# Performance work log

Hardware: AMD Instinct MI355X
Metric: run time of the kernel (lower is better)

Reference implementation:

```python
import jax, jax.numpy as jnp
import numpy as np

ALPHA = 0.9     # projection strength
EPS = 1e-3      # Lyapunov positive-definite regularizer (lyapunov_eps)
B, D, H = 32768, 512, 64


def setup_inputs() -> dict:
    key = jax.random.key(0)
    ks = jax.random.split(key, 8)
    def w(k, shape, fan_in):
        return jax.random.normal(k, shape, jnp.float32) * (1.0 / fan_in) ** 0.5
    return dict(
        x=jax.random.normal(ks[0], (B, D), jnp.float32),
        # dynamics MLP f(x): D -> 64 -> 64 -> D
        W1=w(ks[1], (D, H), D), b1=jnp.zeros((H,), jnp.float32),
        W2=w(ks[2], (H, H), H), b2=jnp.zeros((H,), jnp.float32),
        W3=w(ks[3], (H, D), H), b3=jnp.zeros((D,), jnp.float32),
        # Lyapunov MLP V(z): D -> 64 -> 64 -> 1 (+ eps*||z||^2)
        V1=w(ks[4], (D, H), D), c1=jnp.zeros((H,), jnp.float32),
        V2=w(ks[5], (H, H), H), c2=jnp.zeros((H,), jnp.float32),
        V3=w(ks[6], (H, 1), H), c3=jnp.zeros((1,), jnp.float32),
    )


def reference(x, W1, b1, W2, b2, W3, b3, V1, c1, V2, c2, V3, c3):
    def fnet(xx):  # nominal dynamics: [B,D] -> [B,D]
        h = jax.nn.relu(xx @ W1 + b1)
        h = jax.nn.relu(h @ W2 + b2)
        return h @ W3 + b3

    def vnet(z):  # Lyapunov candidate: [B,D] -> [B]
        h = jax.nn.relu(z @ V1 + c1)
        h = jax.nn.relu(h @ V2 + c2)
        return (h @ V3 + c3)[..., 0] + EPS * jnp.sum(z * z, axis=-1)

    def lyap_sum(xx):
        v = vnet(fnet(xx))
        return jnp.sum(v), v

    # grad_v replicates the in-forward lyapunov.backward(...): dV(f(x))/dx, shape [B,D]
    (_, lyap), grad_v = jax.value_and_grad(lyap_sum, has_aux=True)(x)

    f = fnet(x)                                   # [B, D]
    dot = jnp.sum(grad_v * grad_v, axis=-1)       # bmm(gv, fv): per-sample <grad_v, grad_v>
    denom = jnp.sum(grad_v * grad_v)              # global .pow(2).sum() over all elements
    orth = jax.nn.relu(dot + ALPHA * lyap) / denom  # [B]
    return f - orth[:, None] * grad_v             # diag_embed(orth) @ grad_v
```

## Files before the change

kernel.cpp:

```cpp
#include <hip/hip_runtime.h>

#define ALPHA_C 0.9f
#define EPS_C 1e-3f

typedef unsigned short u16;
typedef __attribute__((ext_vector_type(8))) short short8;
typedef __attribute__((ext_vector_type(4))) short short4v;
typedef __attribute__((ext_vector_type(4))) float f32x4;
#define MFMA(a, b, c) __builtin_amdgcn_mfma_f32_16x16x32_bf16(a, b, c, 0, 0, 0)
#define LDS_FENCE() asm volatile("" ::: "memory")

__device__ __forceinline__ u16 f2bf(float f) {
  union { float f; unsigned u; } v; v.f = f;
  unsigned u = v.u;
  u += 0x7FFFu + ((u >> 16) & 1u);
  return (u16)(u >> 16);
}
__device__ __forceinline__ float bf2f(u16 h) {
  union { unsigned u; float f; } v; v.u = ((unsigned)h) << 16;
  return v.f;
}

__global__ __launch_bounds__(256) void k_conv(
    const float* __restrict__ W1, const float* __restrict__ W2, const float* __restrict__ W3,
    const float* __restrict__ V1, const float* __restrict__ V2,
    u16* __restrict__ PW1T, u16* __restrict__ PW1n, u16* __restrict__ PV1T, u16* __restrict__ PV1n,
    u16* __restrict__ PW3T, u16* __restrict__ PW3n, u16* __restrict__ PW2T, u16* __restrict__ PW2n,
    u16* __restrict__ PV2T, u16* __restrict__ PV2n) {
  int i = blockIdx.x * 256 + threadIdx.x;
  {
    int k = i >> 6, j = i & 63;
    u16 b = f2bf(W1[i]);
    PW1T[((((j >> 4) * 16 + (k >> 5)) * 4 + ((k & 31) >> 3)) * 16 + (j & 15)) * 8 + (k & 7)] = b;
    PW1n[((((k >> 4) * 2 + (j >> 5)) * 4 + ((j & 31) >> 3)) * 16 + (k & 15)) * 8 + (j & 7)] = b;
    u16 c = f2bf(V1[i]);
    PV1T[((((j >> 4) * 16 + (k >> 5)) * 4 + ((k & 31) >> 3)) * 16 + (j & 15)) * 8 + (k & 7)] = c;
    PV1n[((((k >> 4) * 2 + (j >> 5)) * 4 + ((j & 31) >> 3)) * 16 + (k & 15)) * 8 + (j & 7)] = c;
  }
  {
    int k = i >> 9, n = i & 511;
    u16 b = f2bf(W3[i]);
    PW3T[((((n >> 4) * 2 + (k >> 5)) * 4 + ((k & 31) >> 3)) * 16 + (n & 15)) * 8 + (k & 7)] = b;
    PW3n[((((k >> 4) * 16 + (n >> 5)) * 4 + ((n & 31) >> 3)) * 16 + (k & 15)) * 8 + (n & 7)] = b;
  }
  if (i < 4096) {
    int k = i >> 6, j = i & 63;
    u16 b = f2bf(W2[i]);
    PW2T[((((j >> 4) * 2 + (k >> 5)) * 4 + ((k & 31) >> 3)) * 16 + (j & 15)) * 8 + (k & 7)] = b;
    PW2n[((((k >> 4) * 2 + (j >> 5)) * 4 + ((j & 31) >> 3)) * 16 + (k & 15)) * 8 + (j & 7)] = b;
    u16 c = f2bf(V2[i]);
    PV2T[((((j >> 4) * 2 + (k >> 5)) * 4 + ((k & 31) >> 3)) * 16 + (j & 15)) * 8 + (k & 7)] = c;
    PV2n[((((k >> 4) * 2 + (j >> 5)) * 4 + ((j & 31) >> 3)) * 16 + (k & 15)) * 8 + (j & 7)] = c;
  }
}

__global__ __launch_bounds__(256, 2) void k_fused(
    const float* __restrict__ x,
    const u16* __restrict__ PW1T, const float* __restrict__ b1,
    const u16* __restrict__ PW2T, const float* __restrict__ b2,
    const u16* __restrict__ PW3T, const float* __restrict__ b3,
    const u16* __restrict__ PV1T, const float* __restrict__ c1,
    const u16* __restrict__ PV2T, const u16* __restrict__ PV2n, const float* __restrict__ c2,
    const float* __restrict__ V3, const float* __restrict__ c3,
    const u16* __restrict__ PV1n, const u16* __restrict__ PW3n,
    const u16* __restrict__ PW2n, const u16* __restrict__ PW1n,
    u16* __restrict__ FP, u16* __restrict__ T2P,
    float* __restrict__ NUM, float* __restrict__ DP) {
  __shared__ u16 H1s[64 * 72];
  __shared__ u16 H2s[64 * 72];
  __shared__ u16 S2s[64 * 72];
  __shared__ u16 As[64 * 136];
  __shared__ float dred[4];
  const int tid = threadIdx.x;
  const int lane = tid & 63, w = tid >> 6, q = lane >> 4, r = lane & 15;
  const int m0 = blockIdx.x * 64;
  const int arow = w * 16 + r;
  const int strip = blockIdx.x * 4 + w;
  const int h = lane >> 5, c4 = lane & 31;
  const float* xbase = x + (size_t)(m0 + w * 16) * 512;

  f32x4 acc1[4] = {};
  float4 xr0[8], xr1[8];

#define LOAD_X(regs, kc)                                                        \
  _Pragma("unroll") for (int it = 0; it < 8; ++it)                              \
    regs[it] = *(const float4*)&xbase[(it * 2 + h) * 512 + (kc) * 128 + c4 * 4];

#define STAGE_X(regs)                                                           \
  _Pragma("unroll") for (int it = 0; it < 8; ++it) {                            \
    float4 v = regs[it];                                                        \
    short4v s4;                                                                 \
    s4[0] = (short)f2bf(v.x); s4[1] = (short)f2bf(v.y);                         \
    s4[2] = (short)f2bf(v.z); s4[3] = (short)f2bf(v.w);                         \
    *(short4v*)&As[(w * 16 + it * 2 + h) * 136 + c4 * 4] = s4;                  \
  }

#define MFMA_X(kc)                                                              \
  _Pragma("unroll") for (int ks = 0; ks < 4; ++ks) {                            \
    short8 a = *(const short8*)&As[arow * 136 + ks * 32 + q * 8];               \
    _Pragma("unroll") for (int t = 0; t < 4; ++t) {                             \
      short8 b = *(const short8*)&PW1T[((t * 16 + (kc) * 4 + ks) * 64 + lane) * 8]; \
      acc1[t] = MFMA(a, b, acc1[t]);                                            \
    }                                                                           \
  }

  LOAD_X(xr0, 0)
  STAGE_X(xr0) LDS_FENCE(); LOAD_X(xr1, 1) MFMA_X(0) LDS_FENCE();
  STAGE_X(xr1) LDS_FENCE(); LOAD_X(xr0, 2) MFMA_X(1) LDS_FENCE();
  STAGE_X(xr0) LDS_FENCE(); LOAD_X(xr1, 3) MFMA_X(2) LDS_FENCE();
  STAGE_X(xr1) LDS_FENCE(); MFMA_X(3)

  #pragma unroll
  for (int t = 0; t < 4; ++t) {
    int col = t * 16 + r; float bv = b1[col];
    #pragma unroll
    for (int g = 0; g < 4; ++g) {
      float hh = acc1[t][g] + bv; hh = hh > 0.f ? hh : 0.f;
      H1s[(w * 16 + q * 4 + g) * 72 + col] = f2bf(hh);
    }
  }
  LDS_FENCE();

  f32x4 acc2[4] = {};
  #pragma unroll
  for (int ks = 0; ks < 2; ++ks) {
    short8 a = *(const short8*)&H1s[arow * 72 + ks * 32 + q * 8];
    #pragma unroll
    for (int t = 0; t < 4; ++t) {
      short8 b = *(const short8*)&PW2T[((t * 2 + ks) * 64 + lane) * 8];
      acc2[t] = MFMA(a, b, acc2[t]);
    }
  }
  #pragma unroll
  for (int t = 0; t < 4; ++t) {
    int col = t * 16 + r; float bv = b2[col];
    #pragma unroll
    for (int g = 0; g < 4; ++g) {
      float hh = acc2[t][g] + bv; hh = hh > 0.f ? hh : 0.f;
      H2s[(w * 16 + q * 4 + g) * 72 + col] = f2bf(hh);
    }
  }
  LDS_FENCE();

  f32x4 g1acc[4] = {};
  float ssq[4] = {0.f, 0.f, 0.f, 0.f};
  #pragma unroll 1
  for (int nc = 0; nc < 4; ++nc) {
    f32x4 facc[8] = {};
    #pragma unroll
    for (int ks = 0; ks < 2; ++ks) {
      short8 a = *(const short8*)&H2s[arow * 72 + ks * 32 + q * 8];
      #pragma unroll
      for (int t = 0; t < 8; ++t) {
        short8 b = *(const short8*)&PW3T[(((nc * 8 + t) * 2 + ks) * 64 + lane) * 8];
        facc[t] = MFMA(a, b, facc[t]);
      }
    }
    #pragma unroll
    for (int t = 0; t < 8; ++t) {
      float bv = b3[nc * 128 + t * 16 + r];
      short4v s4;
      #pragma unroll
      for (int g = 0; g < 4; ++g) {
        float v = facc[t][g] + bv;
        ssq[g] += v * v;
        u16 bb = f2bf(v);
        As[(w * 16 + q * 4 + g) * 136 + t * 16 + r] = bb;
        s4[g] = (short)bb;
      }
      *(short4v*)&FP[(size_t)(((strip * 4 + nc) * 8 + t) * 64 + lane) * 4] = s4;
    }
    LDS_FENCE();
    #pragma unroll
    for (int ks = 0; ks < 4; ++ks) {
      short8 a = *(const short8*)&As[arow * 136 + ks * 32 + q * 8];
      #pragma unroll
      for (int t = 0; t < 4; ++t) {
        short8 b = *(const short8*)&PV1T[((t * 16 + nc * 4 + ks) * 64 + lane) * 8];
        g1acc[t] = MFMA(a, b, g1acc[t]);
      }
    }
    LDS_FENCE();
  }

  f32x4 g1v[4];
  #pragma unroll
  for (int t = 0; t < 4; ++t) {
    int col = t * 16 + r; float cv = c1[col];
    #pragma unroll
    for (int g = 0; g < 4; ++g) {
      float v = g1acc[t][g] + cv; v = v > 0.f ? v : 0.f;
      g1v[t][g] = v;
      S2s[(w * 16 + q * 4 + g) * 72 + col] = f2bf(v);
    }
  }
  LDS_FENCE();
  f32x4 g2acc[4] = {};
  #pragma unroll
  for (int ks = 0; ks < 2; ++ks) {
    short8 a = *(const short8*)&S2s[arow * 72 + ks * 32 + q * 8];
    #pragma unroll
    for (int t = 0; t < 4; ++t) {
      short8 b = *(const short8*)&PV2T[((t * 2 + ks) * 64 + lane) * 8];
      g2acc[t] = MFMA(a, b, g2acc[t]);
    }
  }
  float tot[4] = {0.f, 0.f, 0.f, 0.f};
  #pragma unroll
  for (int t = 0; t < 4; ++t) {
    int col = t * 16 + r;
    float c2v = c2[col], v3v = V3[col];
    #pragma unroll
    for (int g = 0; g < 4; ++g) {
      float pre = g2acc[t][g] + c2v;
      float g2 = pre > 0.f ? pre : 0.f;
      S2s[(w * 16 + q * 4 + g) * 72 + col] = pre > 0.f ? f2bf(v3v) : (u16)0;
      tot[g] += g2 * v3v;
    }
  }
  LDS_FENCE();
  f32x4 s2acc[4] = {};
  #pragma unroll
  for (int ks = 0; ks < 2; ++ks) {
    short8 a = *(const short8*)&S2s[arow * 72 + ks * 32 + q * 8];
    #pragma unroll
    for (int t = 0; t < 4; ++t) {
      short8 b = *(const short8*)&PV2n[((t * 2 + ks) * 64 + lane) * 8];
      s2acc[t] = MFMA(a, b, s2acc[t]);
    }
  }
  #pragma unroll
  for (int t = 0; t < 4; ++t) {
    int col = t * 16 + r;
    #pragma unroll
    for (int g = 0; g < 4; ++g) {
      float sv = g1v[t][g] > 0.f ? s2acc[t][g] : 0.f;
      S2s[(w * 16 + q * 4 + g) * 72 + col] = f2bf(sv);
    }
  }
  LDS_FENCE();
  float c3v = c3[0];
  float lyap_row[4];
  #pragma unroll
  for (int g = 0; g < 4; ++g) {
    float s = tot[g] + EPS_C * ssq[g];
    s += __shfl_xor(s, 1); s += __shfl_xor(s, 2); s += __shfl_xor(s, 4); s += __shfl_xor(s, 8);
    lyap_row[g] = s + c3v;
  }

  asm volatile("s_waitcnt vmcnt(0)" ::: "memory");

  f32x4 t3acc[4] = {};
  #pragma unroll 1
  for (int nc = 0; nc < 4; ++nc) {
    f32x4 uacc[8] = {};
    #pragma unroll
    for (int ks = 0; ks < 2; ++ks) {
      short8 a = *(const short8*)&S2s[arow * 72 + ks * 32 + q * 8];
      #pragma unroll
      for (int t = 0; t < 8; ++t) {
        short8 b = *(const short8*)&PV1n[(((nc * 8 + t) * 2 + ks) * 64 + lane) * 8];
        uacc[t] = MFMA(a, b, uacc[t]);
      }
    }
    #pragma unroll
    for (int t = 0; t < 8; ++t) {
      short4v f4 = *(const short4v*)&FP[(size_t)(((strip * 4 + nc) * 8 + t) * 64 + lane) * 4];
      #pragma unroll
      for (int g = 0; g < 4; ++g) {
        As[(w * 16 + q * 4 + g) * 136 + t * 16 + r] =
            f2bf(uacc[t][g] + 2.f * EPS_C * bf2f((u16)f4[g]));
      }
    }
    LDS_FENCE();
    #pragma unroll
    for (int ks = 0; ks < 4; ++ks) {
      short8 a = *(const short8*)&As[arow * 136 + ks * 32 + q * 8];
      #pragma unroll
      for (int t = 0; t < 4; ++t) {
        short8 b = *(const short8*)&PW3n[((t * 16 + nc * 4 + ks) * 64 + lane) * 8];
        t3acc[t] = MFMA(a, b, t3acc[t]);
      }
    }
    LDS_FENCE();
  }
  #pragma unroll
  for (int t = 0; t < 4; ++t) {
    int col = t * 16 + r;
    #pragma unroll
    for (int g = 0; g < 4; ++g) {
      int addr = (w * 16 + q * 4 + g) * 72 + col;
      u16 h2 = H2s[addr];
      H2s[addr] = h2 ? f2bf(t3acc[t][g]) : (u16)0;
    }
  }
  LDS_FENCE();
  f32x4 t2acc[4] = {};
  #pragma unroll
  for (int ks = 0; ks < 2; ++ks) {
    short8 a = *(const short8*)&H2s[arow * 72 + ks * 32 + q * 8];
    #pragma unroll
    for (int t = 0; t < 4; ++t) {
      short8 b = *(const short8*)&PW2n[((t * 2 + ks) * 64 + lane) * 8];
      t2acc[t] = MFMA(a, b, t2acc[t]);
    }
  }
  #pragma unroll
  for (int t = 0; t < 4; ++t) {
    int col = t * 16 + r;
    #pragma unroll
    for (int g = 0; g < 4; ++g) {
      int addr = (w * 16 + q * 4 + g) * 72 + col;
      u16 h1 = H1s[addr];
      H1s[addr] = h1 ? f2bf(t2acc[t][g]) : (u16)0;
    }
  }
  LDS_FENCE();
  short8 v0 = *(const short8*)&H1s[arow * 72 + 0 + q * 8];
  short8 v1 = *(const short8*)&H1s[arow * 72 + 32 + q * 8];
  *(short8*)&T2P[(size_t)((strip * 2 + 0) * 64 + lane) * 8] = v0;
  *(short8*)&T2P[(size_t)((strip * 2 + 1) * 64 + lane) * 8] = v1;
  float ssq2[4] = {0.f, 0.f, 0.f, 0.f};
  #pragma unroll 1
  for (int nc = 0; nc < 4; ++nc) {
    f32x4 acc[8] = {};
    #pragma unroll
    for (int t = 0; t < 8; ++t) {
      short8 b0 = *(const short8*)&PW1n[(((nc * 8 + t) * 2 + 0) * 64 + lane) * 8];
      short8 b1 = *(const short8*)&PW1n[(((nc * 8 + t) * 2 + 1) * 64 + lane) * 8];
      acc[t] = MFMA(v0, b0, acc[t]);
      acc[t] = MFMA(v1, b1, acc[t]);
    }
    #pragma unroll
    for (int t = 0; t < 8; ++t)
      #pragma unroll
      for (int g = 0; g < 4; ++g) ssq2[g] += acc[t][g] * acc[t][g];
  }
  float totw = 0.f;
  #pragma unroll
  for (int g = 0; g < 4; ++g) {
    float s = ssq2[g];
    s += __shfl_xor(s, 1); s += __shfl_xor(s, 2); s += __shfl_xor(s, 4); s += __shfl_xor(s, 8);
    if (r == 0) {
      int rowg = m0 + w * 16 + q * 4 + g;
      float nm = s + ALPHA_C * lyap_row[g];
      NUM[rowg] = nm > 0.f ? nm : 0.f;
    }
    s += __shfl_xor(s, 16); s += __shfl_xor(s, 32);
    totw += s;
  }
  if (lane == 0) dred[w] = totw;
  __syncthreads();
  if (tid == 0) atomicAdd(&DP[blockIdx.x & 255], dred[0] + dred[1] + dred[2] + dred[3]);
}

__global__ __launch_bounds__(256) void k_out(
    const u16* __restrict__ T2P, const u16* __restrict__ PW1n,
    const u16* __restrict__ FP, const float* __restrict__ NUM, const float* __restrict__ DP,
    float* __restrict__ out) {
  __shared__ float red[256];
  const int tid = threadIdx.x;
  const int lane = tid & 63, w = tid >> 6, q = lane >> 4, r = lane & 15;
  const int m0 = blockIdx.x * 64;
  const int strip = blockIdx.x * 4 + w;
  red[tid] = DP[tid];
  __syncthreads();
  for (int s = 128; s >= 1; s >>= 1) {
    if (tid < s) red[tid] += red[tid + s];
    __syncthreads();
  }
  const float inv_denom = 1.f / red[0];
  float sc[4];
  #pragma unroll
  for (int g = 0; g < 4; ++g) sc[g] = NUM[m0 + w * 16 + q * 4 + g] * inv_denom;
  short8 a0 = *(const short8*)&T2P[(size_t)((strip * 2 + 0) * 64 + lane) * 8];
  short8 a1 = *(const short8*)&T2P[(size_t)((strip * 2 + 1) * 64 + lane) * 8];
  #pragma unroll 1
  for (int nc = 0; nc < 4; ++nc) {
    f32x4 acc[8] = {};
    #pragma unroll
    for (int t = 0; t < 8; ++t) {
      short8 b0 = *(const short8*)&PW1n[(((nc * 8 + t) * 2 + 0) * 64 + lane) * 8];
      short8 b1 = *(const short8*)&PW1n[(((nc * 8 + t) * 2 + 1) * 64 + lane) * 8];
      acc[t] = MFMA(a0, b0, acc[t]);
      acc[t] = MFMA(a1, b1, acc[t]);
    }
    #pragma unroll
    for (int t = 0; t < 8; ++t) {
      short4v f4 = *(const short4v*)&FP[(size_t)(((strip * 4 + nc) * 8 + t) * 64 + lane) * 4];
      #pragma unroll
      for (int g = 0; g < 4; ++g) {
        out[(size_t)(m0 + w * 16 + q * 4 + g) * 512 + nc * 128 + t * 16 + r] =
            bf2f((u16)f4[g]) - sc[g] * acc[t][g];
      }
    }
  }
}

extern "C" void kernel_launch(void* const* d_in, const int* in_sizes, int n_in,
                              void* d_out, int out_size, void* d_ws, size_t ws_size,
                              hipStream_t stream) {
  const float* x  = (const float*)d_in[0];
  const float* W1 = (const float*)d_in[1];
  const float* b1 = (const float*)d_in[2];
  const float* W2 = (const float*)d_in[3];
  const float* b2 = (const float*)d_in[4];
  const float* W3 = (const float*)d_in[5];
  const float* b3 = (const float*)d_in[6];
  const float* V1 = (const float*)d_in[7];
  const float* c1 = (const float*)d_in[8];
  const float* V2 = (const float*)d_in[9];
  const float* c2 = (const float*)d_in[10];
  const float* V3 = (const float*)d_in[11];
  const float* c3 = (const float*)d_in[12];
  float* out = (float*)d_out;

  u16* FP = (u16*)d_ws;
  float* NUM = (float*)(FP + 16777216);
  float* DP  = NUM + 32768;
  u16* T2P  = (u16*)(DP + 256);
  u16* PW1T = T2P + 2097152;
  u16* PW1n = PW1T + 32768;
  u16* PV1T = PW1n + 32768;
  u16* PV1n = PV1T + 32768;
  u16* PW3T = PV1n + 32768;
  u16* PW3n = PW3T + 32768;
  u16* PW2T = PW3n + 32768;
  u16* PW2n = PW2T + 4096;
  u16* PV2T = PW2n + 4096;
  u16* PV2n = PV2T + 4096;

  hipMemsetAsync(DP, 0, 256 * sizeof(float), stream);

  k_conv<<<128, 256, 0, stream>>>(W1, W2, W3, V1, V2,
                                  PW1T, PW1n, PV1T, PV1n, PW3T, PW3n,
                                  PW2T, PW2n, PV2T, PV2n);
  k_fused<<<512, 256, 0, stream>>>(x, PW1T, b1, PW2T, b2, PW3T, b3, PV1T, c1,
                                   PV2T, PV2n, c2, V3, c3, PV1n, PW3n, PW2n, PW1n,
                                   FP, T2P, NUM, DP);
  k_out<<<512, 256, 0, stream>>>(T2P, PW1n, FP, NUM, DP, out);
}
```

Baseline: 178.3 us.

## Software-pipeline weight fragment loads into registers and stage output stores via LDS

Weight B-fragments for each MFMA stage are prefetched into two rotating register banks (bA/bB), so the global loads for the next chunk are issued while the current chunk's MFMAs run. This applies across all GEMM stages of the fused kernel and to the output kernel. The output kernel also stages results in shared memory so it can write each row with coalesced float4 stores. The DP memset is folded into the weight-conversion kernel, removing one launch. The cost is more registers, which could limit occupancy, plus extra LDS in k_out.

```diff
diff --git a/kernel.cpp b/kernel.cpp
--- a/kernel.cpp
+++ b/kernel.cpp
@@ -26,8 +26,9 @@
     const float* __restrict__ V1, const float* __restrict__ V2,
     u16* __restrict__ PW1T, u16* __restrict__ PW1n, u16* __restrict__ PV1T, u16* __restrict__ PV1n,
     u16* __restrict__ PW3T, u16* __restrict__ PW3n, u16* __restrict__ PW2T, u16* __restrict__ PW2n,
-    u16* __restrict__ PV2T, u16* __restrict__ PV2n) {
+    u16* __restrict__ PV2T, u16* __restrict__ PV2n, float* __restrict__ DP) {
   int i = blockIdx.x * 256 + threadIdx.x;
+  if (i < 256) DP[i] = 0.f;
   {
     int k = i >> 6, j = i & 63;
     u16 b = f2bf(W1[i]);
@@ -53,6 +54,10 @@
     PV2n[((((k >> 4) * 2 + (j >> 5)) * 4 + ((j & 31) >> 3)) * 16 + (k & 15)) * 8 + (j & 7)] = c;
   }
 }
+
+#define LDG8(dst, P, FRAG)                                                      \
+  _Pragma("unroll") for (int j = 0; j < 8; ++j)                                 \
+    dst[j] = *(const short8*)&P[((size_t)(FRAG) * 64 + lane) * 8];
 
 __global__ __launch_bounds__(256, 2) void k_fused(
     const float* __restrict__ x,
@@ -79,36 +84,42 @@
   const int h = lane >> 5, c4 = lane & 31;
   const float* xbase = x + (size_t)(m0 + w * 16) * 512;
 
+  short8 bA[8], bB[8];
+
   f32x4 acc1[4] = {};
-  float4 xr0[8], xr1[8];
-
-#define LOAD_X(regs, kc)                                                        \
-  _Pragma("unroll") for (int it = 0; it < 8; ++it)                              \
-    regs[it] = *(const float4*)&xbase[(it * 2 + h) * 512 + (kc) * 128 + c4 * 4];
-
-#define STAGE_X(regs)                                                           \
-  _Pragma("unroll") for (int it = 0; it < 8; ++it) {                            \
-    float4 v = regs[it];                                                        \
-    short4v s4;                                                                 \
-    s4[0] = (short)f2bf(v.x); s4[1] = (short)f2bf(v.y);                         \
-    s4[2] = (short)f2bf(v.z); s4[3] = (short)f2bf(v.w);                         \
-    *(short4v*)&As[(w * 16 + it * 2 + h) * 136 + c4 * 4] = s4;                  \
-  }
-
-#define MFMA_X(kc)                                                              \
-  _Pragma("unroll") for (int ks = 0; ks < 4; ++ks) {                            \
-    short8 a = *(const short8*)&As[arow * 136 + ks * 32 + q * 8];               \
-    _Pragma("unroll") for (int t = 0; t < 4; ++t) {                             \
-      short8 b = *(const short8*)&PW1T[((t * 16 + (kc) * 4 + ks) * 64 + lane) * 8]; \
-      acc1[t] = MFMA(a, b, acc1[t]);                                            \
+  float4 xr[8];
+  #pragma unroll
+  for (int it = 0; it < 8; ++it)
+    xr[it] = *(const float4*)&xbase[(it * 2 + h) * 512 + c4 * 4];
+  LDG8(bA, PW1T, (j & 3) * 16 + 0 * 4 + (j >> 2));
+
+#define A1_STEP(kc, LAST)                                                       \
+  {                                                                             \
+    _Pragma("unroll") for (int it = 0; it < 8; ++it) {                          \
+      float4 v = xr[it]; short4v s4;                                            \
+      s4[0] = (short)f2bf(v.x); s4[1] = (short)f2bf(v.y);                       \
+      s4[2] = (short)f2bf(v.z); s4[3] = (short)f2bf(v.w);                       \
+      *(short4v*)&As[(w * 16 + it * 2 + h) * 136 + c4 * 4] = s4;                \
     }                                                                           \
-  }
-
-  LOAD_X(xr0, 0)
-  STAGE_X(xr0) LDS_FENCE(); LOAD_X(xr1, 1) MFMA_X(0) LDS_FENCE();
-  STAGE_X(xr1) LDS_FENCE(); LOAD_X(xr0, 2) MFMA_X(1) LDS_FENCE();
-  STAGE_X(xr0) LDS_FENCE(); LOAD_X(xr1, 3) MFMA_X(2) LDS_FENCE();
-  STAGE_X(xr1) LDS_FENCE(); MFMA_X(3)
+    LDS_FENCE();                                                                \
+    if (!LAST) {                                                                \
+      _Pragma("unroll") for (int it = 0; it < 8; ++it)                          \
+        xr[it] = *(const float4*)&xbase[(it * 2 + h) * 512 + (kc + 1) * 128 + c4 * 4]; \
+    }                                                                           \
+    LDG8(bB, PW1T, (j & 3) * 16 + (kc) * 4 + 2 + (j >> 2));       \
+    short8 a0 = *(const short8*)&As[arow * 136 + 0 * 32 + q * 8];               \
+    short8 a1 = *(const short8*)&As[arow * 136 + 1 * 32 + q * 8];               \
+    _Pragma("unroll") for (int t = 0; t < 4; ++t) acc1[t] = MFMA(a0, bA[t], acc1[t]); \
+    _Pragma("unroll") for (int t = 0; t < 4; ++t) acc1[t] = MFMA(a1, bA[4 + t], acc1[t]); \
+    if (!LAST) { LDG8(bA, PW1T, (j & 3) * 16 + (kc + 1) * 4 + (j >> 2)); }      \
+    else       { LDG8(bA, PW2T, (j & 3) * 2 + (j >> 2)); }        \
+    short8 a2 = *(const short8*)&As[arow * 136 + 2 * 32 + q * 8];               \
+    short8 a3 = *(const short8*)&As[arow * 136 + 3 * 32 + q * 8];               \
+    _Pragma("unroll") for (int t = 0; t < 4; ++t) acc1[t] = MFMA(a2, bB[t], acc1[t]); \
+    _Pragma("unroll") for (int t = 0; t < 4; ++t) acc1[t] = MFMA(a3, bB[4 + t], acc1[t]); \
+  }
+
+  A1_STEP(0, 0) A1_STEP(1, 0) A1_STEP(2, 0) A1_STEP(3, 1)
 
   #pragma unroll
   for (int t = 0; t < 4; ++t) {
@@ -121,41 +132,45 @@
   }
   LDS_FENCE();
 
-  f32x4 acc2[4] = {};
-  #pragma unroll
-  for (int ks = 0; ks < 2; ++ks) {
-    short8 a = *(const short8*)&H1s[arow * 72 + ks * 32 + q * 8];
+  {
+    short8 a0 = *(const short8*)&H1s[arow * 72 + 0 + q * 8];
+    short8 a1 = *(const short8*)&H1s[arow * 72 + 32 + q * 8];
+    f32x4 acc2[4] = {};
+    #pragma unroll
+    for (int t = 0; t < 4; ++t) acc2[t] = MFMA(a0, bA[t], acc2[t]);
+    LDG8(bB, PW3T, ((j & 3)) * 2 + (j >> 2));
+    #pragma unroll
+    for (int t = 0; t < 4; ++t) acc2[t] = MFMA(a1, bA[4 + t], acc2[t]);
     #pragma unroll
     for (int t = 0; t < 4; ++t) {
-      short8 b = *(const short8*)&PW2T[((t * 2 + ks) * 64 + lane) * 8];
-      acc2[t] = MFMA(a, b, acc2[t]);
-    }
-  }
-  #pragma unroll
-  for (int t = 0; t < 4; ++t) {
-    int col = t * 16 + r; float bv = b2[col];
-    #pragma unroll
-    for (int g = 0; g < 4; ++g) {
-      float hh = acc2[t][g] + bv; hh = hh > 0.f ? hh : 0.f;
-      H2s[(w * 16 + q * 4 + g) * 72 + col] = f2bf(hh);
+      int col = t * 16 + r; float bv = b2[col];
+      #pragma unroll
+      for (int g = 0; g < 4; ++g) {
+        float hh = acc2[t][g] + bv; hh = hh > 0.f ? hh : 0.f;
+        H2s[(w * 16 + q * 4 + g) * 72 + col] = f2bf(hh);
+      }
     }
   }
   LDS_FENCE();
 
   f32x4 g1acc[4] = {};
   float ssq[4] = {0.f, 0.f, 0.f, 0.f};
+  short8 h2a0 = *(const short8*)&H2s[arow * 72 + 0 + q * 8];
+  short8 h2a1 = *(const short8*)&H2s[arow * 72 + 32 + q * 8];
   #pragma unroll 1
   for (int nc = 0; nc < 4; ++nc) {
+    LDG8(bA, PW3T, ((nc * 8 + 4 + (j & 3)) * 2 + (j >> 2)));
     f32x4 facc[8] = {};
     #pragma unroll
-    for (int ks = 0; ks < 2; ++ks) {
-      short8 a = *(const short8*)&H2s[arow * 72 + ks * 32 + q * 8];
-      #pragma unroll
-      for (int t = 0; t < 8; ++t) {
-        short8 b = *(const short8*)&PW3T[(((nc * 8 + t) * 2 + ks) * 64 + lane) * 8];
-        facc[t] = MFMA(a, b, facc[t]);
-      }
-    }
+    for (int t = 0; t < 4; ++t) facc[t] = MFMA(h2a0, bB[t], facc[t]);
+    #pragma unroll
+    for (int t = 0; t < 4; ++t) facc[t] = MFMA(h2a1, bB[4 + t], facc[t]);
+    LDG8(bB, PV1T, ((j & 3) * 16 + nc * 4 + (j >> 2)));
+    #pragma unroll
+    for (int t = 0; t < 4; ++t) facc[4 + t] = MFMA(h2a0, bA[t], facc[4 + t]);
+    #pragma unroll
+    for (int t = 0; t < 4; ++t) facc[4 + t] = MFMA(h2a1, bA[4 + t], facc[4 + t]);
+    LDG8(bA, PV1T, ((j & 3) * 16 + nc * 4 + 2 + (j >> 2)));
     #pragma unroll
     for (int t = 0; t < 8; ++t) {
       float bv = b3[nc * 128 + t * 16 + r];
@@ -171,15 +186,20 @@
       *(short4v*)&FP[(size_t)(((strip * 4 + nc) * 8 + t) * 64 + lane) * 4] = s4;
     }
     LDS_FENCE();
-    #pragma unroll
-    for (int ks = 0; ks < 4; ++ks) {
-      short8 a = *(const short8*)&As[arow * 136 + ks * 32 + q * 8];
-      #pragma unroll
-      for (int t = 0; t < 4; ++t) {
-        short8 b = *(const short8*)&PV1T[((t * 16 + nc * 4 + ks) * 64 + lane) * 8];
-        g1acc[t] = MFMA(a, b, g1acc[t]);
-      }
-    }
+    short8 a0 = *(const short8*)&As[arow * 136 + 0 * 32 + q * 8];
+    short8 a1 = *(const short8*)&As[arow * 136 + 1 * 32 + q * 8];
+    #pragma unroll
+    for (int t = 0; t < 4; ++t) g1acc[t] = MFMA(a0, bB[t], g1acc[t]);
+    #pragma unroll
+    for (int t = 0; t < 4; ++t) g1acc[t] = MFMA(a1, bB[4 + t], g1acc[t]);
+    int ncn = (nc + 1) & 3;
+    LDG8(bB, PW3T, ((ncn * 8 + (j & 3)) * 2 + (j >> 2)));
+    short8 a2 = *(const short8*)&As[arow * 136 + 2 * 32 + q * 8];
+    short8 a3 = *(const short8*)&As[arow * 136 + 3 * 32 + q * 8];
+    #pragma unroll
+    for (int t = 0; t < 4; ++t) g1acc[t] = MFMA(a2, bA[t], g1acc[t]);
+    #pragma unroll
+    for (int t = 0; t < 4; ++t) g1acc[t] = MFMA(a3, bA[4 + t], g1acc[t]);
     LDS_FENCE();
   }
 
@@ -194,16 +214,16 @@
       S2s[(w * 16 + q * 4 + g) * 72 + col] = f2bf(v);
     }
   }
+  LDG8(bA, PV2T, (j & 3) * 2 + (j >> 2));
   LDS_FENCE();
   f32x4 g2acc[4] = {};
-  #pragma unroll
-  for (int ks = 0; ks < 2; ++ks) {
-    short8 a = *(const short8*)&S2s[arow * 72 + ks * 32 + q * 8];
-    #pragma unroll
-    for (int t = 0; t < 4; ++t) {
-      short8 b = *(const short8*)&PV2T[((t * 2 + ks) * 64 + lane) * 8];
-      g2acc[t] = MFMA(a, b, g2acc[t]);
-    }
+  {
+    short8 a0 = *(const short8*)&S2s[arow * 72 + 0 + q * 8];
+    short8 a1 = *(const short8*)&S2s[arow * 72 + 32 + q * 8];
+    #pragma unroll
+    for (int t = 0; t < 4; ++t) g2acc[t] = MFMA(a0, bA[t], g2acc[t]);
+    #pragma unroll
+    for (int t = 0; t < 4; ++t) g2acc[t] = MFMA(a1, bA[4 + t], g2acc[t]);
   }
   float tot[4] = {0.f, 0.f, 0.f, 0.f};
   #pragma unroll
@@ -218,16 +238,16 @@
       tot[g] += g2 * v3v;
     }
   }
+  LDG8(bB, PV2n, (j & 3) * 2 + (j >> 2));
   LDS_FENCE();
   f32x4 s2acc[4] = {};
-  #pragma unroll
-  for (int ks = 0; ks < 2; ++ks) {
-    short8 a = *(const short8*)&S2s[arow * 72 + ks * 32 + q * 8];
-    #pragma unroll
-    for (int t = 0; t < 4; ++t) {
-      short8 b = *(const short8*)&PV2n[((t * 2 + ks) * 64 + lane) * 8];
-      s2acc[t] = MFMA(a, b, s2acc[t]);
-    }
+  {
+    short8 a0 = *(const short8*)&S2s[arow * 72 + 0 + q * 8];
+    short8 a1 = *(const short8*)&S2s[arow * 72 + 32 + q * 8];
+    #pragma unroll
+    for (int t = 0; t < 4; ++t) s2acc[t] = MFMA(a0, bB[t], s2acc[t]);
+    #pragma unroll
+    for (int t = 0; t < 4; ++t) s2acc[t] = MFMA(a1, bB[4 + t], s2acc[t]);
   }
   #pragma unroll
   for (int t = 0; t < 4; ++t) {
@@ -251,37 +271,50 @@
   asm volatile("s_waitcnt vmcnt(0)" ::: "memory");
 
   f32x4 t3acc[4] = {};
+  short8 s2a0 = *(const short8*)&S2s[arow * 72 + 0 + q * 8];
+  short8 s2a1 = *(const short8*)&S2s[arow * 72 + 32 + q * 8];
+  LDG8(bA, PV1n, (((j & 3)) * 2 + (j >> 2)));
   #pragma unroll 1
   for (int nc = 0; nc < 4; ++nc) {
+    LDG8(bB, PV1n, ((nc * 8 + 4 + (j & 3)) * 2 + (j >> 2)));
+    short4v fpr[8];
+    #pragma unroll
+    for (int t = 0; t < 8; ++t)
+      fpr[t] = *(const short4v*)&FP[(size_t)(((strip * 4 + nc) * 8 + t) * 64 + lane) * 4];
     f32x4 uacc[8] = {};
     #pragma unroll
-    for (int ks = 0; ks < 2; ++ks) {
-      short8 a = *(const short8*)&S2s[arow * 72 + ks * 32 + q * 8];
-      #pragma unroll
-      for (int t = 0; t < 8; ++t) {
-        short8 b = *(const short8*)&PV1n[(((nc * 8 + t) * 2 + ks) * 64 + lane) * 8];
-        uacc[t] = MFMA(a, b, uacc[t]);
-      }
-    }
+    for (int t = 0; t < 4; ++t) uacc[t] = MFMA(s2a0, bA[t], uacc[t]);
+    #pragma unroll
+    for (int t = 0; t < 4; ++t) uacc[t] = MFMA(s2a1, bA[4 + t], uacc[t]);
+    LDG8(bA, PW3n, ((j & 3) * 16 + nc * 4 + (j >> 2)));
+    #pragma unroll
+    for (int t = 0; t < 4; ++t) uacc[4 + t] = MFMA(s2a0, bB[t], uacc[4 + t]);
+    #pragma unroll
+    for (int t = 0; t < 4; ++t) uacc[4 + t] = MFMA(s2a1, bB[4 + t], uacc[4 + t]);
+    LDG8(bB, PW3n, ((j & 3) * 16 + nc * 4 + 2 + (j >> 2)));
     #pragma unroll
     for (int t = 0; t < 8; ++t) {
-      short4v f4 = *(const short4v*)&FP[(size_t)(((strip * 4 + nc) * 8 + t) * 64 + lane) * 4];
       #pragma unroll
       for (int g = 0; g < 4; ++g) {
         As[(w * 16 + q * 4 + g) * 136 + t * 16 + r] =
-            f2bf(uacc[t][g] + 2.f * EPS_C * bf2f((u16)f4[g]));
+            f2bf(uacc[t][g] + 2.f * EPS_C * bf2f((u16)fpr[t][g]));
       }
     }
     LDS_FENCE();
-    #pragma unroll
-    for (int ks = 0; ks < 4; ++ks) {
-      short8 a = *(const short8*)&As[arow * 136 + ks * 32 + q * 8];
-      #pragma unroll
-      for (int t = 0; t < 4; ++t) {
-        short8 b = *(const short8*)&PW3n[((t * 16 + nc * 4 + ks) * 64 + lane) * 8];
-        t3acc[t] = MFMA(a, b, t3acc[t]);
-      }
-    }
+    short8 a0 = *(const short8*)&As[arow * 136 + 0 * 32 + q * 8];
+    short8 a1 = *(const short8*)&As[arow * 136 + 1 * 32 + q * 8];
+    #pragma unroll
+    for (int t = 0; t < 4; ++t) t3acc[t] = MFMA(a0, bA[t], t3acc[t]);
+    #pragma unroll
+    for (int t = 0; t < 4; ++t) t3acc[t] = MFMA(a1, bA[4 + t], t3acc[t]);
+    int ncn = (nc + 1) & 3;
+    LDG8(bA, PV1n, ((ncn * 8 + (j & 3)) * 2 + (j >> 2)));
+    short8 a2 = *(const short8*)&As[arow * 136 + 2 * 32 + q * 8];
+    short8 a3 = *(const short8*)&As[arow * 136 + 3 * 32 + q * 8];
+    #pragma unroll
+    for (int t = 0; t < 4; ++t) t3acc[t] = MFMA(a2, bB[t], t3acc[t]);
+    #pragma unroll
+    for (int t = 0; t < 4; ++t) t3acc[t] = MFMA(a3, bB[4 + t], t3acc[t]);
     LDS_FENCE();
   }
   #pragma unroll
@@ -294,16 +327,16 @@
       H2s[addr] = h2 ? f2bf(t3acc[t][g]) : (u16)0;
     }
   }
+  LDG8(bB, PW2n, (j & 3) * 2 + (j >> 2));
   LDS_FENCE();
   f32x4 t2acc[4] = {};
-  #pragma unroll
-  for (int ks = 0; ks < 2; ++ks) {
-    short8 a = *(const short8*)&H2s[arow * 72 + ks * 32 + q * 8];
-    #pragma unroll
-    for (int t = 0; t < 4; ++t) {
-      short8 b = *(const short8*)&PW2n[((t * 2 + ks) * 64 + lane) * 8];
-      t2acc[t] = MFMA(a, b, t2acc[t]);
-    }
+  {
+    short8 a0 = *(const short8*)&H2s[arow * 72 + 0 + q * 8];
+    short8 a1 = *(const short8*)&H2s[arow * 72 + 32 + q * 8];
+    #pragma unroll
+    for (int t = 0; t < 4; ++t) t2acc[t] = MFMA(a0, bB[t], t2acc[t]);
+    #pragma unroll
+    for (int t = 0; t < 4; ++t) t2acc[t] = MFMA(a1, bB[4 + t], t2acc[t]);
   }
   #pragma unroll
   for (int t = 0; t < 4; ++t) {
@@ -315,6 +348,7 @@
       H1s[addr] = h1 ? f2bf(t2acc[t][g]) : (u16)0;
     }
   }
+  LDG8(bA, PW1n, ((j >> 1) * 2 + (j & 1)));
   LDS_FENCE();
   short8 v0 = *(const short8*)&H1s[arow * 72 + 0 + q * 8];
   short8 v1 = *(const short8*)&H1s[arow * 72 + 32 + q * 8];
@@ -323,13 +357,19 @@
   float ssq2[4] = {0.f, 0.f, 0.f, 0.f};
   #pragma unroll 1
   for (int nc = 0; nc < 4; ++nc) {
+    LDG8(bB, PW1n, ((nc * 8 + 4 + (j >> 1)) * 2 + (j & 1)));
     f32x4 acc[8] = {};
     #pragma unroll
-    for (int t = 0; t < 8; ++t) {
-      short8 b0 = *(const short8*)&PW1n[(((nc * 8 + t) * 2 + 0) * 64 + lane) * 8];
-      short8 b1 = *(const short8*)&PW1n[(((nc * 8 + t) * 2 + 1) * 64 + lane) * 8];
-      acc[t] = MFMA(v0, b0, acc[t]);
-      acc[t] = MFMA(v1, b1, acc[t]);
+    for (int t = 0; t < 4; ++t) {
+      acc[t] = MFMA(v0, bA[t * 2 + 0], acc[t]);
+      acc[t] = MFMA(v1, bA[t * 2 + 1], acc[t]);
+    }
+    int ncn = (nc + 1) & 3;
+    LDG8(bA, PW1n, ((ncn * 8 + (j >> 1)) * 2 + (j & 1)));
+    #pragma unroll
+    for (int t = 0; t < 4; ++t) {
+      acc[4 + t] = MFMA(v0, bB[t * 2 + 0], acc[4 + t]);
+      acc[4 + t] = MFMA(v1, bB[t * 2 + 1], acc[4 + t]);
     }
     #pragma unroll
     for (int t = 0; t < 8; ++t)
@@ -354,11 +394,12 @@
   if (tid == 0) atomicAdd(&DP[blockIdx.x & 255], dred[0] + dred[1] + dred[2] + dred[3]);
 }
 
-__global__ __launch_bounds__(256) void k_out(
+__global__ __launch_bounds__(256, 2) void k_out(
     const u16* __restrict__ T2P, const u16* __restrict__ PW1n,
     const u16* __restrict__ FP, const float* __restrict__ NUM, const float* __restrict__ DP,
     float* __restrict__ out) {
   __shared__ float red[256];
+  __shared__ float OutS[64 * 132];
   const int tid = threadIdx.x;
   const int lane = tid & 63, w = tid >> 6, q = lane >> 4, r = lane & 15;
   const int m0 = blockIdx.x * 64;
@@ -375,25 +416,42 @@
   for (int g = 0; g < 4; ++g) sc[g] = NUM[m0 + w * 16 + q * 4 + g] * inv_denom;
   short8 a0 = *(const short8*)&T2P[(size_t)((strip * 2 + 0) * 64 + lane) * 8];
   short8 a1 = *(const short8*)&T2P[(size_t)((strip * 2 + 1) * 64 + lane) * 8];
+  short8 bA[8], bB[8];
+  LDG8(bA, PW1n, ((j >> 1) * 2 + (j & 1)));
   #pragma unroll 1
   for (int nc = 0; nc < 4; ++nc) {
+    LDG8(bB, PW1n, ((nc * 8 + 4 + (j >> 1)) * 2 + (j & 1)));
+    short4v fpr[8];
+    #pragma unroll
+    for (int t = 0; t < 8; ++t)
+      fpr[t] = *(const short4v*)&FP[(size_t)(((strip * 4 + nc) * 8 + t) * 64 + lane) * 4];
     f32x4 acc[8] = {};
     #pragma unroll
+    for (int t = 0; t < 4; ++t) {
+      acc[t] = MFMA(a0, bA[t * 2 + 0], acc[t]);
+      acc[t] = MFMA(a1, bA[t * 2 + 1], acc[t]);
+    }
+    int ncn = (nc + 1) & 3;
+    LDG8(bA, PW1n, ((ncn * 8 + (j >> 1)) * 2 + (j & 1)));
+    #pragma unroll
+    for (int t = 0; t < 4; ++t) {
+      acc[4 + t] = MFMA(a0, bB[t * 2 + 0], acc[4 + t]);
+      acc[4 + t] = MFMA(a1, bB[t * 2 + 1], acc[4 + t]);
+    }
+    #pragma unroll
     for (int t = 0; t < 8; ++t) {
-      short8 b0 = *(const short8*)&PW1n[(((nc * 8 + t) * 2 + 0) * 64 + lane) * 8];
-      short8 b1 = *(const short8*)&PW1n[(((nc * 8 + t) * 2 + 1) * 64 + lane) * 8];
-      acc[t] = MFMA(a0, b0, acc[t]);
-      acc[t] = MFMA(a1, b1, acc[t]);
-    }
-    #pragma unroll
-    for (int t = 0; t < 8; ++t) {
-      short4v f4 = *(const short4v*)&FP[(size_t)(((strip * 4 + nc) * 8 + t) * 64 + lane) * 4];
       #pragma unroll
-      for (int g = 0; g < 4; ++g) {
-        out[(size_t)(m0 + w * 16 + q * 4 + g) * 512 + nc * 128 + t * 16 + r] =
-            bf2f((u16)f4[g]) - sc[g] * acc[t][g];
-      }
-    }
+      for (int g = 0; g < 4; ++g)
+        OutS[(w * 16 + q * 4 + g) * 132 + t * 16 + r] =
+            bf2f((u16)fpr[t][g]) - sc[g] * acc[t][g];
+    }
+    LDS_FENCE();
+    #pragma unroll
+    for (int jj = 0; jj < 8; ++jj) {
+      f32x4 ov = *(const f32x4*)&OutS[(w * 16 + (lane >> 5) + jj * 2) * 132 + (lane & 31) * 4];
+      *(f32x4*)&out[(size_t)(m0 + w * 16 + (lane >> 5) + jj * 2) * 512 + nc * 128 + (lane & 31) * 4] = ov;
+    }
+    LDS_FENCE();
   }
 }
 
@@ -430,11 +488,9 @@
   u16* PV2T = PW2n + 4096;
   u16* PV2n = PV2T + 4096;
 
-  hipMemsetAsync(DP, 0, 256 * sizeof(float), stream);
-
   k_conv<<<128, 256, 0, stream>>>(W1, W2, W3, V1, V2,
                                   PW1T, PW1n, PV1T, PV1n, PW3T, PW3n,
-                                  PW2T, PW2n, PV2T, PV2n);
+                                  PW2T, PW2n, PV2T, PV2n, DP);
   k_fused<<<512, 256, 0, stream>>>(x, PW1T, b1, PW2T, b2, PW3T, b3, PV1T, c1,
                                    PV2T, PV2n, c2, V3, c3, PV1n, PW3n, PW2n, PW1n,
                                    FP, T2P, NUM, DP);
```

After: 178.1 us. About the same (-0.1%).
